# Kernel optimization log

Hardware: AMD Instinct MI355X
Metric: run time of the kernel (lower is better)

## Reference

```python
import jax, jax.numpy as jnp
import numpy as np

CHUNK = 32
EPS = 1e-6

def _l2norm(x):
    return x * jax.lax.rsqrt(jnp.sum(x * x, axis=-1, keepdims=True) + EPS)

def setup_inputs() -> dict:
    key = jax.random.key(0)
    k1, k2, k3, k4 = jax.random.split(key, 4)
    b, h, L, dk, dv = 4, 8, 4096, 128, 128
    return {
        'q': jax.random.normal(k1, (b, h, L, dk), dtype=jnp.float32),
        'k': jax.random.normal(k2, (b, h, L, dk), dtype=jnp.float32),
        'v': jax.random.normal(k3, (b, h, L, dv), dtype=jnp.float32),
        'beta': jax.random.uniform(k4, (b, h, L), dtype=jnp.float32),
    }

def _delta_rule_chunkwise(q, k, v, beta):
    b, h, L, dk = q.shape
    dv = v.shape[-1]
    c = CHUNK
    assert L % c == 0, 'L must be a multiple of chunk_size (no padding path)'
    n = L // c

    q = _l2norm(q)
    k = _l2norm(k)
    v = v * beta[..., None]
    k_beta = k * beta[..., None]

    # [b,h,n,c,d]
    resh = lambda t: t.reshape(b, h, n, c, t.shape[-1])
    qc, kc, vc, kbc = resh(q), resh(k), resh(v), resh(k_beta)

    ones = jnp.ones((c, c), dtype=jnp.float32)
    strict_lower = jnp.tril(ones, -1)      # below diagonal
    lower_inc = jnp.tril(ones, 0)          # diagonal and below

    # inv = -(k_beta @ k^T) with upper-incl-diag zeroed, then forward substitution
    inv = -jnp.einsum('bhncd,bhned->bhnce', kbc, kc) * strict_lower
    for i in range(1, c):
        # inv[..., i, :i] += inv[..., i, :] @ inv[..., :, :i]
        upd = jnp.einsum('bhnk,bhnkj->bhnj', inv[..., i, :], inv[..., :, :i])
        inv = inv.at[..., i, :i].add(upd)
    inv = inv + jnp.eye(c, dtype=inv.dtype)

    u = jnp.einsum('bhnce,bhned->bhncd', inv, vc)    # [b,h,n,c,dv]
    w = jnp.einsum('bhnce,bhned->bhncd', inv, kbc)   # [b,h,n,c,dk]

    # scan over chunks carrying state S [b,h,dk,dv]
    def step(S, inp):
        q_i, k_i, u0_i, w_i = inp  # [b,h,c,d*]
        attn = jnp.einsum('bhcd,bhed->bhce', q_i, k_i) * lower_inc
        u_i = u0_i - jnp.einsum('bhcd,bhdv->bhcv', w_i, S)
        out_i = jnp.einsum('bhcd,bhdv->bhcv', q_i, S) + jnp.einsum('bhce,bhev->bhcv', attn, u_i)
        S = S + jnp.einsum('bhcd,bhcv->bhdv', k_i, u_i)
        return S, out_i

    chunk_first = lambda t: jnp.moveaxis(t, 2, 0)  # [n,b,h,c,d]
    S0 = jnp.zeros((b, h, dk, dv), dtype=q.dtype)
    S, out = jax.lax.scan(step, S0, (chunk_first(qc), chunk_first(kc), chunk_first(u), chunk_first(w)))
    out = jnp.moveaxis(out, 0, 2).reshape(b, h, L, dv)
    return out, S

def reference(q, k, v, beta):
    out, S = _delta_rule_chunkwise(q, k, v, beta)
    return out
```

## Files before the change

### kernel.cpp

```cpp
#include <hip/hip_runtime.h>
#include <math.h>

#define CHUNK 32
#define DK 128
#define DV 128
#define L_SEQ 4096
#define BH 32
#define NCH 128

typedef __attribute__((ext_vector_type(8))) short bf16x8;
typedef __attribute__((ext_vector_type(4))) float f32x4;

union U8 { unsigned int u[4]; bf16x8 v; };

#define MFMA16(a, b, c) __builtin_amdgcn_mfma_f32_16x16x32_bf16((a), (b), (c), 0, 0, 0)
#define LGKM_WAIT() __asm__ __volatile__("s_waitcnt lgkmcnt(0)" ::: "memory")

__device__ __forceinline__ unsigned short f2bf(float x){
    unsigned int u = __builtin_bit_cast(unsigned int, x);
    u = u + 0x7FFFu + ((u >> 16) & 1u);
    return (unsigned short)(u >> 16);
}
__device__ __forceinline__ unsigned int pk2(float a, float b){
    unsigned int r;
    asm("v_cvt_pk_bf16_f32 %0, %1, %2" : "=v"(r) : "v"(a), "v"(b));
    return r;
}

__device__ __forceinline__ bf16x8 afragF32(const float (*M)[36], int row, int q8){
    float4 f0 = *(const float4*)&M[row][q8];
    float4 f1 = *(const float4*)&M[row][q8 + 4];
    U8 t;
    t.u[0] = pk2(f0.x, f0.y); t.u[1] = pk2(f0.z, f0.w);
    t.u[2] = pk2(f1.x, f1.y); t.u[3] = pk2(f1.z, f1.w);
    return t.v;
}
__device__ __forceinline__ bf16x8 bfragF32(const float (*M)[36], int q8, int col){
    U8 t;
#pragma unroll
    for (int j2 = 0; j2 < 4; ++j2)
        t.u[j2] = pk2(M[q8 + 2*j2][col], M[q8 + 2*j2 + 1][col]);
    return t.v;
}


__global__ __launch_bounds__(64, 1)
void prep_kernel(const float* __restrict__ q, const float* __restrict__ k,
                 const float* __restrict__ beta,
                 unsigned short* __restrict__ qw, unsigned short* __restrict__ kw,
                 unsigned short* __restrict__ Tw, unsigned short* __restrict__ Aw)
{
    const int bc = blockIdx.x;
    const size_t row0 = (size_t)bc * CHUNK;
    const int l = threadIdx.x;
    const int r = l & 31, h = l >> 5;
    const int quad = (l >> 4) & 3, ln15 = l & 15, q8 = quad * 8;

    __shared__ unsigned short qn_s[32][136], kn_s[32][136], kb_s[32][136];
    __shared__ float Ms[32][36];
    __shared__ float Rs[32][36];

    const float bet = beta[row0 + r];

    {
        const float4* gp = (const float4*)(q + (row0 + r) * DK + 64 * h);
        float vb[64]; float s = 0.f;
#pragma unroll
        for (int e = 0; e < 16; ++e){
            float4 a = gp[e];
            vb[4*e+0]=a.x; vb[4*e+1]=a.y; vb[4*e+2]=a.z; vb[4*e+3]=a.w;
            s += a.x*a.x + a.y*a.y + a.z*a.z + a.w*a.w;
        }
        s += __shfl_xor(s, 32);
        float sc = rsqrtf(s + 1e-6f);
#pragma unroll
        for (int e = 0; e < 8; ++e){
            U8 t;
#pragma unroll
            for (int j = 0; j < 4; ++j)
                t.u[j] = pk2(vb[8*e+2*j] * sc, vb[8*e+2*j+1] * sc);
            *(bf16x8*)&qn_s[r][64*h + 8*e] = t.v;
            *(bf16x8*)(qw + (row0 + r) * DK + 64*h + 8*e) = t.v;
        }
    }
    {
        const float4* gp = (const float4*)(k + (row0 + r) * DK + 64 * h);
        float vb[64]; float s = 0.f;
#pragma unroll
        for (int e = 0; e < 16; ++e){
            float4 a = gp[e];
            vb[4*e+0]=a.x; vb[4*e+1]=a.y; vb[4*e+2]=a.z; vb[4*e+3]=a.w;
            s += a.x*a.x + a.y*a.y + a.z*a.z + a.w*a.w;
        }
        s += __shfl_xor(s, 32);
        float sc = rsqrtf(s + 1e-6f);
#pragma unroll
        for (int e = 0; e < 8; ++e){
            U8 t, tb;
#pragma unroll
            for (int j = 0; j < 4; ++j){
                float x0 = vb[8*e+2*j] * sc, x1 = vb[8*e+2*j+1] * sc;
                t.u[j]  = pk2(x0, x1);
                tb.u[j] = pk2(x0 * bet, x1 * bet);
            }
            *(bf16x8*)&kn_s[r][64*h + 8*e] = t.v;
            *(bf16x8*)&kb_s[r][64*h + 8*e] = tb.v;
            *(bf16x8*)(kw + (row0 + r) * DK + 64*h + 8*e) = t.v;
        }
    }
    LGKM_WAIT();

    f32x4 Z = {0.f, 0.f, 0.f, 0.f};
    f32x4 Bacc[2][2] = {{Z, Z}, {Z, Z}};
    f32x4 Aacc[2][2] = {{Z, Z}, {Z, Z}};
#pragma unroll
    for (int ks = 0; ks < 4; ++ks){
        bf16x8 bF[2];
        bF[0] = *(const bf16x8*)&kn_s[ln15][32*ks + q8];
        bF[1] = *(const bf16x8*)&kn_s[16 + ln15][32*ks + q8];
#pragma unroll
        for (int mt = 0; mt < 2; ++mt){
            bf16x8 aK = *(const bf16x8*)&kb_s[16*mt + ln15][32*ks + q8];
            bf16x8 aQ = *(const bf16x8*)&qn_s[16*mt + ln15][32*ks + q8];
#pragma unroll
            for (int nt = 0; nt < 2; ++nt){
                Bacc[mt][nt] = MFMA16(aK, bF[nt], Bacc[mt][nt]);
                Aacc[mt][nt] = MFMA16(aQ, bF[nt], Aacc[mt][nt]);
            }
        }
    }

    f32x4 Rc[2][2];
#pragma unroll
    for (int mt = 0; mt < 2; ++mt)
#pragma unroll
    for (int nt = 0; nt < 2; ++nt)
#pragma unroll
    for (int rg = 0; rg < 4; ++rg){
        int row = 16*mt + 4*quad + rg, col = 16*nt + ln15;
        float av = (col <= row) ? Aacc[mt][nt][rg] : 0.f;
        Aw[((size_t)bc << 10) + row*32 + col] = f2bf(av);
        float bm = (col < row) ? -Bacc[mt][nt][rg] : 0.f;
        Ms[row][col] = bm;
        Rc[mt][nt][rg] = bm + ((col == row) ? 1.f : 0.f);
    }

#pragma unroll 1
    for (int rd = 0; rd < 4; ++rd){
        LGKM_WAIT();
        bf16x8 Am[2], Bm2[2];
#pragma unroll
        for (int mt = 0; mt < 2; ++mt) Am[mt] = afragF32(Ms, 16*mt + ln15, q8);
#pragma unroll
        for (int nt = 0; nt < 2; ++nt) Bm2[nt] = bfragF32(Ms, q8, 16*nt + ln15);
        f32x4 Mq[2][2];
#pragma unroll
        for (int mt = 0; mt < 2; ++mt)
#pragma unroll
        for (int nt = 0; nt < 2; ++nt)
            Mq[mt][nt] = MFMA16(Am[mt], Bm2[nt], Z);
#pragma unroll
        for (int mt = 0; mt < 2; ++mt)
#pragma unroll
        for (int nt = 0; nt < 2; ++nt)
#pragma unroll
        for (int rg = 0; rg < 4; ++rg){
            int row = 16*mt + 4*quad + rg, col = 16*nt + ln15;
            Rs[row][col] = Rc[mt][nt][rg];
            Ms[row][col] = Mq[mt][nt][rg];
        }
        LGKM_WAIT();
        bf16x8 Ar[2], Bq[2];
#pragma unroll
        for (int mt = 0; mt < 2; ++mt) Ar[mt] = afragF32(Rs, 16*mt + ln15, q8);
#pragma unroll
        for (int nt = 0; nt < 2; ++nt) Bq[nt] = bfragF32(Ms, q8, 16*nt + ln15);
#pragma unroll
        for (int mt = 0; mt < 2; ++mt)
#pragma unroll
        for (int nt = 0; nt < 2; ++nt)
            Rc[mt][nt] = MFMA16(Ar[mt], Bq[nt], Rc[mt][nt]);
    }

#pragma unroll
    for (int mt = 0; mt < 2; ++mt)
#pragma unroll
    for (int nt = 0; nt < 2; ++nt)
#pragma unroll
    for (int rg = 0; rg < 4; ++rg){
        int row = 16*mt + 4*quad + rg, col = 16*nt + ln15;
        Tw[((size_t)bc << 10) + row*32 + col] = f2bf(Rc[mt][nt][rg]);
    }
}


__global__ __launch_bounds__(64, 1)
void scan_kernel(const float* __restrict__ v, const float* __restrict__ beta,
                 const unsigned short* __restrict__ qw, const unsigned short* __restrict__ kw,
                 const unsigned short* __restrict__ Tw, const unsigned short* __restrict__ Aw,
                 float* __restrict__ out)
{
    const int id = blockIdx.x;
    const int bh = id & 31, cb = id >> 5, c0 = cb * 16;
    const int l = threadIdx.x;
    const int quad = (l >> 4) & 3, ln15 = l & 15, q8 = quad * 8;
    const int hi = l >> 5;

    __shared__ unsigned short knR[4392];
    __shared__ unsigned short Xt[16][40];
    __shared__ unsigned short ut[16][40];

    const f32x4 Z = {0.f, 0.f, 0.f, 0.f};
    f32x4 Sacc[8];
#pragma unroll
    for (int t = 0; t < 8; ++t) Sacc[t] = Z;

    const size_t bhL = (size_t)bh * L_SEQ;
    const int a0 = (((l & 16) << 1) | ln15) << 2;
    const int a1 = a0 + 64;

    bf16x8 kAa[2][4], kAb[2][4];
    bf16x8 qA[2][4], tA[2], aA[2], knA[8], uB;
    float vr[8], br[8];

    auto loadK = [&](int ch, bf16x8 (&kA)[2][4]){
        const unsigned short* kp = kw + (bhL + (size_t)ch * CHUNK) * DK;
#pragma unroll
        for (int mt = 0; mt < 2; ++mt)
#pragma unroll
        for (int ks = 0; ks < 4; ++ks)
            kA[mt][ks] = *(const bf16x8*)(kp + (16*mt + ln15) * DK + 32*ks + q8);
    };
    auto loadQ = [&](int ch){
        const unsigned short* qp = qw + (bhL + (size_t)ch * CHUNK) * DK;
#pragma unroll
        for (int mt = 0; mt < 2; ++mt)
#pragma unroll
        for (int ks = 0; ks < 4; ++ks)
            qA[mt][ks] = *(const bf16x8*)(qp + (16*mt + ln15) * DK + 32*ks + q8);
    };
    auto loadT = [&](int ch){
        const unsigned short* Tp = Tw + ((size_t)(bh * NCH + ch) << 10);
#pragma unroll
        for (int mt = 0; mt < 2; ++mt)
            tA[mt] = *(const bf16x8*)(Tp + (16*mt + ln15) * 32 + q8);
    };
    auto loadA = [&](int ch){
        const unsigned short* Ap = Aw + ((size_t)(bh * NCH + ch) << 10);
#pragma unroll
        for (int mt = 0; mt < 2; ++mt)
            aA[mt] = *(const bf16x8*)(Ap + (16*mt + ln15) * 32 + q8);
    };
    auto loadVB = [&](int ch){
        const size_t row0 = bhL + (size_t)ch * CHUNK;
#pragma unroll
        for (int g = 0; g < 8; ++g){
            int i = 16*(g >> 2) + 4*quad + (g & 3);
            vr[g] = v[(row0 + i) * DV + c0 + ln15];
            br[g] = beta[row0 + i];
        }
    };

    loadK(0, kAa);
    loadQ(0); loadT(0); loadA(0); loadVB(0);
    loadK(1, kAb);
    {
        U8 z; z.u[0] = 0u; z.u[1] = 0u; z.u[2] = 0u; z.u[3] = 0u;
        uB = z.v;
#pragma unroll
        for (int t = 0; t < 8; ++t) knA[t] = z.v;
    }

    auto body = [&](int ch, bf16x8 (&cur)[2][4]){
        const size_t row0 = bhL + (size_t)ch * CHUNK;

#pragma unroll
        for (int t = 0; t < 8; ++t)
            Sacc[t] = MFMA16(knA[t], uB, Sacc[t]);

        int P[8][2];
#pragma unroll
        for (int t = 0; t < 8; ++t){
            P[t][0] = (int)pk2(Sacc[t][0], Sacc[t][1]);
            P[t][1] = (int)pk2(Sacc[t][2], Sacc[t][3]);
        }
        bf16x8 SB[4];
#pragma unroll
        for (int ks = 0; ks < 4; ++ks){
            U8 sb;
            int e, f;
            e = __builtin_amdgcn_ds_bpermute(a0, P[2*ks][0]);
            f = __builtin_amdgcn_ds_bpermute(a0, P[2*ks+1][0]);
            sb.u[0] = (unsigned)(hi ? f : e);
            e = __builtin_amdgcn_ds_bpermute(a0, P[2*ks][1]);
            f = __builtin_amdgcn_ds_bpermute(a0, P[2*ks+1][1]);
            sb.u[1] = (unsigned)(hi ? f : e);
            e = __builtin_amdgcn_ds_bpermute(a1, P[2*ks][0]);
            f = __builtin_amdgcn_ds_bpermute(a1, P[2*ks+1][0]);
            sb.u[2] = (unsigned)(hi ? f : e);
            e = __builtin_amdgcn_ds_bpermute(a1, P[2*ks][1]);
            f = __builtin_amdgcn_ds_bpermute(a1, P[2*ks+1][1]);
            sb.u[3] = (unsigned)(hi ? f : e);
            SB[ks] = sb.v;
        }

        f32x4 Y[2] = {Z, Z}, Op[2] = {Z, Z};
#pragma unroll
        for (int ks = 0; ks < 4; ++ks)
#pragma unroll
        for (int mt = 0; mt < 2; ++mt){
            Y[mt]  = MFMA16(cur[mt][ks], SB[ks], Y[mt]);
            Op[mt] = MFMA16(qA[mt][ks],  SB[ks], Op[mt]);
        }

#pragma unroll
        for (int mt = 0; mt < 2; ++mt){
            unsigned int w0 = pk2(br[4*mt+0] * (vr[4*mt+0] - Y[mt][0]),
                                  br[4*mt+1] * (vr[4*mt+1] - Y[mt][1]));
            unsigned int w1 = pk2(br[4*mt+2] * (vr[4*mt+2] - Y[mt][2]),
                                  br[4*mt+3] * (vr[4*mt+3] - Y[mt][3]));
            *(unsigned int*)&Xt[ln15][16*mt + 4*quad]     = w0;
            *(unsigned int*)&Xt[ln15][16*mt + 4*quad + 2] = w1;
        }

#pragma unroll
        for (int mt = 0; mt < 2; ++mt)
#pragma unroll
        for (int ks = 0; ks < 4; ++ks){
            int i = 16*mt + ln15;
            int ad = i * 136 + (i >> 3) * 16 + 32*ks + q8;
            *(bf16x8*)&knR[ad] = cur[mt][ks];
        }

        bf16x8 Xb = *(const bf16x8*)&Xt[ln15][q8];

        unsigned int rja[32];
#pragma unroll
        for (int t = 0; t < 4; ++t)
#pragma unroll
        for (int j = 0; j < 8; ++j)
            rja[8*t + j] = knR[(q8 + j) * 136 + ((q8 + j) >> 3) * 16 + 16*t + ln15];

        f32x4 U[2];
#pragma unroll
        for (int mt = 0; mt < 2; ++mt) U[mt] = MFMA16(tA[mt], Xb, Z);

#pragma unroll
        for (int mt = 0; mt < 2; ++mt){
            *(unsigned int*)&ut[ln15][16*mt + 4*quad]     = pk2(U[mt][0], U[mt][1]);
            *(unsigned int*)&ut[ln15][16*mt + 4*quad + 2] = pk2(U[mt][2], U[mt][3]);
        }

#pragma unroll
        for (int t = 0; t < 4; ++t){
            U8 kk;
            kk.u[0] = rja[8*t+0] | (rja[8*t+1] << 16);
            kk.u[1] = rja[8*t+2] | (rja[8*t+3] << 16);
            kk.u[2] = rja[8*t+4] | (rja[8*t+5] << 16);
            kk.u[3] = rja[8*t+6] | (rja[8*t+7] << 16);
            knA[t] = kk.v;
        }

        uB = *(const bf16x8*)&ut[ln15][q8];

        const int chn = (ch + 1 < NCH) ? ch + 1 : NCH - 1;
        const int ch2 = (ch + 2 < NCH) ? ch + 2 : NCH - 1;
        loadQ(chn); loadT(chn); loadVB(chn);
        loadK(ch2, cur);

        unsigned int rjb[32];
#pragma unroll
        for (int t = 0; t < 4; ++t)
#pragma unroll
        for (int j = 0; j < 8; ++j)
            rjb[8*t + j] = knR[(q8 + j) * 136 + ((q8 + j) >> 3) * 16 + 16*(t + 4) + ln15];

        f32x4 O[2];
#pragma unroll
        for (int mt = 0; mt < 2; ++mt) O[mt] = MFMA16(aA[mt], uB, Op[mt]);
#pragma unroll
        for (int mt = 0; mt < 2; ++mt)
#pragma unroll
        for (int rg = 0; rg < 4; ++rg)
            out[(row0 + 16*mt + 4*quad + rg) * DV + c0 + ln15] = O[mt][rg];

#pragma unroll
        for (int t = 0; t < 4; ++t){
            U8 kk;
            kk.u[0] = rjb[8*t+0] | (rjb[8*t+1] << 16);
            kk.u[1] = rjb[8*t+2] | (rjb[8*t+3] << 16);
            kk.u[2] = rjb[8*t+4] | (rjb[8*t+5] << 16);
            kk.u[3] = rjb[8*t+6] | (rjb[8*t+7] << 16);
            knA[t + 4] = kk.v;
        }
        loadA(chn);
    };

    for (int ch = 0; ch < NCH; ch += 2){
        body(ch,     kAa);
        body(ch + 1, kAb);
    }
}


__global__ __launch_bounds__(512, 1)
void deltanet_fused(const float* __restrict__ q, const float* __restrict__ k,
                    const float* __restrict__ v, const float* __restrict__ beta,
                    float* __restrict__ out)
{
    const int bh = blockIdx.x;
    const int tid = threadIdx.x;
    const int n = L_SEQ / CHUNK;

    __shared__ float S[DK][DV + 1];
    __shared__ float qs[CHUNK][DK + 1];
    __shared__ float ks[CHUNK][DK + 1];
    __shared__ float vs[CHUNK][DV + 1];
    __shared__ float kbs[CHUNK][DK + 1];
    __shared__ float T[CHUNK][CHUNK + 1];
    __shared__ float at[CHUNK][CHUNK + 1];
    __shared__ float bet[CHUNK];

    for (int idx = tid; idx < DK * DV; idx += 512)
        S[idx / DV][idx % DV] = 0.f;
    __syncthreads();

    const size_t base_bh = (size_t)bh * L_SEQ;

    for (int ch = 0; ch < n; ++ch){
        const size_t row0 = base_bh + (size_t)ch * CHUNK;
        for (int idx = tid; idx < CHUNK * DK; idx += 512){
            int r = idx >> 7, c = idx & 127;
            size_t g = (row0 + (size_t)r) * DK + c;
            qs[r][c] = q[g]; ks[r][c] = k[g]; vs[r][c] = v[g];
        }
        if (tid < CHUNK) bet[tid] = beta[row0 + tid];
        __syncthreads();
        if (tid < 64){
            int r = tid & 31;
            const float* src = (tid < 32) ? &qs[r][0] : &ks[r][0];
            float s = 0.f;
            for (int d = 0; d < DK; ++d){ float x = src[d]; s += x * x; }
            at[(tid < 32) ? 0 : 1][r] = 1.0f / sqrtf(s + 1e-6f);
        }
        __syncthreads();
        for (int idx = tid; idx < CHUNK * DK; idx += 512){
            int r = idx >> 7, c = idx & 127;
            float qq = qs[r][c] * at[0][r];
            float kk = ks[r][c] * at[1][r];
            float b = bet[r];
            qs[r][c] = qq; ks[r][c] = kk; kbs[r][c] = kk * b; vs[r][c] *= b;
        }
        __syncthreads();
        for (int idx = tid; idx < CHUNK * CHUNK; idx += 512){
            int i = idx >> 5, j = idx & 31;
            float s = 0.f;
            if (j < i){
                for (int d = 0; d < DK; ++d) s += kbs[i][d] * ks[j][d];
                s = -s;
            }
            T[i][j] = s;
        }
        __syncthreads();
        for (int i = 1; i < CHUNK; ++i){
            float upd = 0.f;
            if (tid < i){
                int j = tid;
                for (int kk = j + 1; kk < i; ++kk) upd += T[i][kk] * T[kk][j];
            }
            __syncthreads();
            if (tid < i) T[i][tid] += upd;
            __syncthreads();
        }
        if (tid < CHUNK) T[tid][tid] = 1.0f;
        __syncthreads();
        {
            int c = tid & 127;
            int i0 = (tid >> 7) * 8;
            float uacc[8], wacc[8];
#pragma unroll
            for (int r = 0; r < 8; ++r){ uacc[r] = 0.f; wacc[r] = 0.f; }
            for (int j = 0; j < CHUNK; ++j){
                float vvv = vs[j][c], kb = kbs[j][c];
#pragma unroll
                for (int r = 0; r < 8; ++r){
                    float tt = T[i0 + r][j];
                    uacc[r] += tt * vvv; wacc[r] += tt * kb;
                }
            }
            __syncthreads();
#pragma unroll
            for (int r = 0; r < 8; ++r){ vs[i0 + r][c] = uacc[r]; kbs[i0 + r][c] = wacc[r]; }
        }
        __syncthreads();
        for (int idx = tid; idx < CHUNK * CHUNK; idx += 512){
            int i = idx >> 5, j = idx & 31;
            float s = 0.f;
            if (j <= i) for (int d = 0; d < DK; ++d) s += qs[i][d] * ks[j][d];
            at[i][j] = s;
        }
        __syncthreads();
        {
            int c = tid & 127;
            int i0 = (tid >> 7) * 8;
            float acc[8];
#pragma unroll
            for (int r = 0; r < 8; ++r) acc[r] = 0.f;
            for (int d = 0; d < DK; ++d){
                float sv = S[d][c];
#pragma unroll
                for (int r = 0; r < 8; ++r) acc[r] += kbs[i0 + r][d] * sv;
            }
#pragma unroll
            for (int r = 0; r < 8; ++r) vs[i0 + r][c] -= acc[r];
        }
        __syncthreads();
        {
            int c = tid & 127;
            int i0 = (tid >> 7) * 8;
            float acc[8];
#pragma unroll
            for (int r = 0; r < 8; ++r) acc[r] = 0.f;
            for (int d = 0; d < DK; ++d){
                float sv = S[d][c];
#pragma unroll
                for (int r = 0; r < 8; ++r) acc[r] += qs[i0 + r][d] * sv;
            }
            for (int j = 0; j < CHUNK; ++j){
                float uv = vs[j][c];
#pragma unroll
                for (int r = 0; r < 8; ++r) acc[r] += at[i0 + r][j] * uv;
            }
#pragma unroll
            for (int r = 0; r < 8; ++r)
                out[(row0 + (size_t)(i0 + r)) * DV + c] = acc[r];
        }
        __syncthreads();
        {
            int c = tid & 127;
            int d0 = (tid >> 7) * 32;
            float acc[32];
#pragma unroll
            for (int r = 0; r < 32; ++r) acc[r] = 0.f;
            for (int i = 0; i < CHUNK; ++i){
                float uv = vs[i][c];
#pragma unroll
                for (int r = 0; r < 32; ++r) acc[r] += ks[i][d0 + r] * uv;
            }
#pragma unroll
            for (int r = 0; r < 32; ++r) S[d0 + r][c] += acc[r];
        }
        __syncthreads();
    }
}

extern "C" void kernel_launch(void* const* d_in, const int* in_sizes, int n_in,
                              void* d_out, int out_size, void* d_ws, size_t ws_size,
                              hipStream_t stream) {
    const float* q = (const float*)d_in[0];
    const float* k = (const float*)d_in[1];
    const float* v = (const float*)d_in[2];
    const float* beta = (const float*)d_in[3];
    float* out = (float*)d_out;

    const size_t QK = (size_t)BH * L_SEQ * DK;
    const size_t TA = (size_t)BH * NCH * 1024;
    const size_t need = (2 * QK + 2 * TA) * sizeof(unsigned short);

    if (ws_size >= need){
        unsigned short* qwp = (unsigned short*)d_ws;
        unsigned short* kwp = qwp + QK;
        unsigned short* Twp = kwp + QK;
        unsigned short* Awp = Twp + TA;
        prep_kernel<<<BH * NCH, 64, 0, stream>>>(q, k, beta, qwp, kwp, Twp, Awp);
        scan_kernel<<<BH * 8, 64, 0, stream>>>(v, beta, qwp, kwp, Twp, Awp, out);
    } else {
        deltanet_fused<<<BH, 512, 0, stream>>>(q, k, v, beta, out);
    }
}
```

Before: 368.9 us.

## Add register-resident scan kernel with pre-transposed K from prep

The prep kernel now loads q/k straight into MFMA fragment registers instead of staging them in LDS. It also writes an extra transposed bf16 copy of normalized k per chunk. A new scan_fast kernel keeps the state S in MFMA accumulators, moves fragments between lanes with ds_bpermute instead of shared memory, and prefetches the next chunk's operands during the current one. This aims to cut LDS traffic and barriers in the serial chunk scan, at the cost of more workspace and extra global writes and reads for the transposed K, and it only runs when the workspace is large enough.

```diff
diff --git a/kernel.cpp b/kernel.cpp
--- a/kernel.cpp
+++ b/kernel.cpp
@@ -44,90 +44,127 @@
 }
 
 
-__global__ __launch_bounds__(64, 1)
+template<bool WKT>
+__global__ __launch_bounds__(64)
 void prep_kernel(const float* __restrict__ q, const float* __restrict__ k,
                  const float* __restrict__ beta,
                  unsigned short* __restrict__ qw, unsigned short* __restrict__ kw,
-                 unsigned short* __restrict__ Tw, unsigned short* __restrict__ Aw)
+                 unsigned short* __restrict__ Tw, unsigned short* __restrict__ Aw,
+                 unsigned short* __restrict__ kwT)
 {
     const int bc = blockIdx.x;
     const size_t row0 = (size_t)bc * CHUNK;
     const int l = threadIdx.x;
-    const int r = l & 31, h = l >> 5;
     const int quad = (l >> 4) & 3, ln15 = l & 15, q8 = quad * 8;
 
-    __shared__ unsigned short qn_s[32][136], kn_s[32][136], kb_s[32][136];
     __shared__ float Ms[32][36];
     __shared__ float Rs[32][36];
-
-    const float bet = beta[row0 + r];
-
+    __shared__ unsigned short knS[WKT ? 4392 : 2];
+
+    const float bet0 = beta[row0 + ln15];
+    const float bet1 = beta[row0 + 16 + ln15];
+
+    bf16x8 qF[2][4];
     {
-        const float4* gp = (const float4*)(q + (row0 + r) * DK + 64 * h);
-        float vb[64]; float s = 0.f;
-#pragma unroll
-        for (int e = 0; e < 16; ++e){
-            float4 a = gp[e];
-            vb[4*e+0]=a.x; vb[4*e+1]=a.y; vb[4*e+2]=a.z; vb[4*e+3]=a.w;
-            s += a.x*a.x + a.y*a.y + a.z*a.z + a.w*a.w;
-        }
-        s += __shfl_xor(s, 32);
-        float sc = rsqrtf(s + 1e-6f);
-#pragma unroll
-        for (int e = 0; e < 8; ++e){
-            U8 t;
-#pragma unroll
-            for (int j = 0; j < 4; ++j)
-                t.u[j] = pk2(vb[8*e+2*j] * sc, vb[8*e+2*j+1] * sc);
-            *(bf16x8*)&qn_s[r][64*h + 8*e] = t.v;
-            *(bf16x8*)(qw + (row0 + r) * DK + 64*h + 8*e) = t.v;
-        }
-    }
+        float4 raw[2][4][2];
+        float s0 = 0.f, s1 = 0.f;
+#pragma unroll
+        for (int mt = 0; mt < 2; ++mt)
+#pragma unroll
+        for (int ks = 0; ks < 4; ++ks){
+            const float* p = q + (row0 + 16*mt + ln15) * DK + 32*ks + q8;
+            raw[mt][ks][0] = *(const float4*)p;
+            raw[mt][ks][1] = *(const float4*)(p + 4);
+        }
+#pragma unroll
+        for (int ks = 0; ks < 4; ++ks)
+#pragma unroll
+        for (int h = 0; h < 2; ++h){
+            float4 a = raw[0][ks][h], b = raw[1][ks][h];
+            s0 += a.x*a.x + a.y*a.y + a.z*a.z + a.w*a.w;
+            s1 += b.x*b.x + b.y*b.y + b.z*b.z + b.w*b.w;
+        }
+        s0 += __shfl_xor(s0, 16); s0 += __shfl_xor(s0, 32);
+        s1 += __shfl_xor(s1, 16); s1 += __shfl_xor(s1, 32);
+        float sc0 = rsqrtf(s0 + 1e-6f), sc1 = rsqrtf(s1 + 1e-6f);
+#pragma unroll
+        for (int mt = 0; mt < 2; ++mt){
+            float sc = mt ? sc1 : sc0;
+#pragma unroll
+            for (int ks = 0; ks < 4; ++ks){
+                float4 a = raw[mt][ks][0], b = raw[mt][ks][1];
+                U8 t;
+                t.u[0] = pk2(a.x*sc, a.y*sc); t.u[1] = pk2(a.z*sc, a.w*sc);
+                t.u[2] = pk2(b.x*sc, b.y*sc); t.u[3] = pk2(b.z*sc, b.w*sc);
+                qF[mt][ks] = t.v;
+                *(bf16x8*)(qw + (row0 + 16*mt + ln15) * DK + 32*ks + q8) = t.v;
+            }
+        }
+    }
+    bf16x8 kF[2][4], kB[2][4];
     {
-        const float4* gp = (const float4*)(k + (row0 + r) * DK + 64 * h);
-        float vb[64]; float s = 0.f;
-#pragma unroll
-        for (int e = 0; e < 16; ++e){
-            float4 a = gp[e];
-            vb[4*e+0]=a.x; vb[4*e+1]=a.y; vb[4*e+2]=a.z; vb[4*e+3]=a.w;
-            s += a.x*a.x + a.y*a.y + a.z*a.z + a.w*a.w;
-        }
-        s += __shfl_xor(s, 32);
-        float sc = rsqrtf(s + 1e-6f);
-#pragma unroll
-        for (int e = 0; e < 8; ++e){
-            U8 t, tb;
-#pragma unroll
-            for (int j = 0; j < 4; ++j){
-                float x0 = vb[8*e+2*j] * sc, x1 = vb[8*e+2*j+1] * sc;
-                t.u[j]  = pk2(x0, x1);
-                tb.u[j] = pk2(x0 * bet, x1 * bet);
+        float4 raw[2][4][2];
+        float s0 = 0.f, s1 = 0.f;
+#pragma unroll
+        for (int mt = 0; mt < 2; ++mt)
+#pragma unroll
+        for (int ks = 0; ks < 4; ++ks){
+            const float* p = k + (row0 + 16*mt + ln15) * DK + 32*ks + q8;
+            raw[mt][ks][0] = *(const float4*)p;
+            raw[mt][ks][1] = *(const float4*)(p + 4);
+        }
+#pragma unroll
+        for (int ks = 0; ks < 4; ++ks)
+#pragma unroll
+        for (int h = 0; h < 2; ++h){
+            float4 a = raw[0][ks][h], b = raw[1][ks][h];
+            s0 += a.x*a.x + a.y*a.y + a.z*a.z + a.w*a.w;
+            s1 += b.x*b.x + b.y*b.y + b.z*b.z + b.w*b.w;
+        }
+        s0 += __shfl_xor(s0, 16); s0 += __shfl_xor(s0, 32);
+        s1 += __shfl_xor(s1, 16); s1 += __shfl_xor(s1, 32);
+        float sc0 = rsqrtf(s0 + 1e-6f), sc1 = rsqrtf(s1 + 1e-6f);
+#pragma unroll
+        for (int mt = 0; mt < 2; ++mt){
+            float sc = mt ? sc1 : sc0;
+            float bb = mt ? bet1 : bet0;
+#pragma unroll
+            for (int ks = 0; ks < 4; ++ks){
+                float4 a = raw[mt][ks][0], b = raw[mt][ks][1];
+                float x0=a.x*sc, x1=a.y*sc, x2=a.z*sc, x3=a.w*sc;
+                float x4=b.x*sc, x5=b.y*sc, x6=b.z*sc, x7=b.w*sc;
+                U8 t, tb;
+                t.u[0]=pk2(x0,x1); t.u[1]=pk2(x2,x3); t.u[2]=pk2(x4,x5); t.u[3]=pk2(x6,x7);
+                tb.u[0]=pk2(x0*bb,x1*bb); tb.u[1]=pk2(x2*bb,x3*bb);
+                tb.u[2]=pk2(x4*bb,x5*bb); tb.u[3]=pk2(x6*bb,x7*bb);
+                kF[mt][ks] = t.v; kB[mt][ks] = tb.v;
+                *(bf16x8*)(kw + (row0 + 16*mt + ln15) * DK + 32*ks + q8) = t.v;
             }
-            *(bf16x8*)&kn_s[r][64*h + 8*e] = t.v;
-            *(bf16x8*)&kb_s[r][64*h + 8*e] = tb.v;
-            *(bf16x8*)(kw + (row0 + r) * DK + 64*h + 8*e) = t.v;
-        }
-    }
-    LGKM_WAIT();
+        }
+    }
+
+    if constexpr (WKT){
+#pragma unroll
+        for (int mt = 0; mt < 2; ++mt)
+#pragma unroll
+        for (int ks = 0; ks < 4; ++ks){
+            int i = 16*mt + ln15;
+            int ad = i * 136 + (i >> 3) * 16 + 32*ks + q8;
+            *(bf16x8*)&knS[ad] = kF[mt][ks];
+        }
+    }
 
     f32x4 Z = {0.f, 0.f, 0.f, 0.f};
     f32x4 Bacc[2][2] = {{Z, Z}, {Z, Z}};
     f32x4 Aacc[2][2] = {{Z, Z}, {Z, Z}};
 #pragma unroll
-    for (int ks = 0; ks < 4; ++ks){
-        bf16x8 bF[2];
-        bF[0] = *(const bf16x8*)&kn_s[ln15][32*ks + q8];
-        bF[1] = *(const bf16x8*)&kn_s[16 + ln15][32*ks + q8];
-#pragma unroll
-        for (int mt = 0; mt < 2; ++mt){
-            bf16x8 aK = *(const bf16x8*)&kb_s[16*mt + ln15][32*ks + q8];
-            bf16x8 aQ = *(const bf16x8*)&qn_s[16*mt + ln15][32*ks + q8];
-#pragma unroll
-            for (int nt = 0; nt < 2; ++nt){
-                Bacc[mt][nt] = MFMA16(aK, bF[nt], Bacc[mt][nt]);
-                Aacc[mt][nt] = MFMA16(aQ, bF[nt], Aacc[mt][nt]);
-            }
-        }
+    for (int ks = 0; ks < 4; ++ks)
+#pragma unroll
+    for (int mt = 0; mt < 2; ++mt)
+#pragma unroll
+    for (int nt = 0; nt < 2; ++nt){
+        Bacc[mt][nt] = MFMA16(kB[mt][ks], kF[nt][ks], Bacc[mt][nt]);
+        Aacc[mt][nt] = MFMA16(qF[mt][ks], kF[nt][ks], Aacc[mt][nt]);
     }
 
     f32x4 Rc[2][2];
@@ -145,6 +182,23 @@
         Rc[mt][nt][rg] = bm + ((col == row) ? 1.f : 0.f);
     }
 
+    if constexpr (WKT){
+        unsigned short* kT = kwT + ((size_t)bc << 12);
+#pragma unroll
+        for (int t = 0; t < 8; ++t){
+            unsigned short rj[8];
+#pragma unroll
+            for (int j = 0; j < 8; ++j)
+                rj[j] = knS[(q8 + j) * 136 + ((q8 + j) >> 3) * 16 + 16*t + ln15];
+            U8 kk;
+            kk.u[0] = (unsigned)rj[0] | ((unsigned)rj[1] << 16);
+            kk.u[1] = (unsigned)rj[2] | ((unsigned)rj[3] << 16);
+            kk.u[2] = (unsigned)rj[4] | ((unsigned)rj[5] << 16);
+            kk.u[3] = (unsigned)rj[6] | ((unsigned)rj[7] << 16);
+            *(bf16x8*)(kT + (16*t + ln15) * 32 + q8) = kk.v;
+        }
+    }
+
 #pragma unroll 1
     for (int rd = 0; rd < 4; ++rd){
         LGKM_WAIT();
@@ -190,6 +244,166 @@
     for (int rg = 0; rg < 4; ++rg){
         int row = 16*mt + 4*quad + rg, col = 16*nt + ln15;
         Tw[((size_t)bc << 10) + row*32 + col] = f2bf(Rc[mt][nt][rg]);
+    }
+}
+
+
+__global__ __launch_bounds__(64, 1)
+void scan_fast(const float* __restrict__ v, const float* __restrict__ beta,
+               const unsigned short* __restrict__ qw, const unsigned short* __restrict__ kw,
+               const unsigned short* __restrict__ kwT,
+               const unsigned short* __restrict__ Tw, const unsigned short* __restrict__ Aw,
+               float* __restrict__ out)
+{
+    const int id = blockIdx.x;
+    const int bh = id & 31, cb = id >> 5, c0 = cb * 16;
+    const int l = threadIdx.x;
+    const int quad = (l >> 4) & 3, ln15 = l & 15, q8 = quad * 8;
+    const int hi = l >> 5;
+
+    const f32x4 Z = {0.f, 0.f, 0.f, 0.f};
+    f32x4 Sacc[8];
+#pragma unroll
+    for (int t = 0; t < 8; ++t) Sacc[t] = Z;
+
+    const size_t bhL = (size_t)bh * L_SEQ;
+    const int a0 = (((l & 16) << 1) | ln15) << 2;
+    const int a1 = a0 + 64;
+
+    bf16x8 cur[2][4], qA[2][4], knA[8], tA[2], aA[2], uB;
+    float vr[8], br[8];
+
+    auto quadswap = [&](int p0, int p1, int p2, int p3) -> bf16x8 {
+        U8 r; int e, f;
+        e = __builtin_amdgcn_ds_bpermute(a0, p0); f = __builtin_amdgcn_ds_bpermute(a0, p2);
+        r.u[0] = (unsigned)(hi ? f : e);
+        e = __builtin_amdgcn_ds_bpermute(a0, p1); f = __builtin_amdgcn_ds_bpermute(a0, p3);
+        r.u[1] = (unsigned)(hi ? f : e);
+        e = __builtin_amdgcn_ds_bpermute(a1, p0); f = __builtin_amdgcn_ds_bpermute(a1, p2);
+        r.u[2] = (unsigned)(hi ? f : e);
+        e = __builtin_amdgcn_ds_bpermute(a1, p1); f = __builtin_amdgcn_ds_bpermute(a1, p3);
+        r.u[3] = (unsigned)(hi ? f : e);
+        return r.v;
+    };
+
+    auto loadK = [&](int ch){
+        const unsigned short* kp = kw + (bhL + (size_t)ch * CHUNK) * DK;
+#pragma unroll
+        for (int mt = 0; mt < 2; ++mt)
+#pragma unroll
+        for (int ks = 0; ks < 4; ++ks)
+            cur[mt][ks] = *(const bf16x8*)(kp + (16*mt + ln15) * DK + 32*ks + q8);
+    };
+    auto loadQ = [&](int ch){
+        const unsigned short* qp = qw + (bhL + (size_t)ch * CHUNK) * DK;
+#pragma unroll
+        for (int mt = 0; mt < 2; ++mt)
+#pragma unroll
+        for (int ks = 0; ks < 4; ++ks)
+            qA[mt][ks] = *(const bf16x8*)(qp + (16*mt + ln15) * DK + 32*ks + q8);
+    };
+    auto loadT = [&](int ch){
+        const unsigned short* Tp = Tw + ((size_t)(bh * NCH + ch) << 10);
+#pragma unroll
+        for (int mt = 0; mt < 2; ++mt)
+            tA[mt] = *(const bf16x8*)(Tp + (16*mt + ln15) * 32 + q8);
+    };
+    auto loadA = [&](int ch){
+        const unsigned short* Ap = Aw + ((size_t)(bh * NCH + ch) << 10);
+#pragma unroll
+        for (int mt = 0; mt < 2; ++mt)
+            aA[mt] = *(const bf16x8*)(Ap + (16*mt + ln15) * 32 + q8);
+    };
+    auto loadVB = [&](int ch){
+        const size_t row0 = bhL + (size_t)ch * CHUNK;
+#pragma unroll
+        for (int g = 0; g < 8; ++g){
+            int i = 16*(g >> 2) + 4*quad + (g & 3);
+            vr[g] = v[(row0 + i) * DV + c0 + ln15];
+            br[g] = beta[row0 + i];
+        }
+    };
+    auto loadKT = [&](int ch){
+        const unsigned short* p = kwT + ((size_t)(bh * NCH + ch) << 12);
+#pragma unroll
+        for (int t = 0; t < 8; ++t)
+            knA[t] = *(const bf16x8*)(p + (16*t + ln15) * 32 + q8);
+    };
+
+    loadK(0); loadQ(0); loadT(0); loadA(0); loadVB(0);
+    {
+        U8 z; z.u[0] = 0u; z.u[1] = 0u; z.u[2] = 0u; z.u[3] = 0u;
+        uB = z.v;
+#pragma unroll
+        for (int t = 0; t < 8; ++t) knA[t] = z.v;
+    }
+
+    for (int ch = 0; ch < NCH; ++ch){
+        const size_t row0 = bhL + (size_t)ch * CHUNK;
+        const int chn = (ch + 1 < NCH) ? ch + 1 : NCH - 1;
+
+#pragma unroll
+        for (int t = 0; t < 8; ++t)
+            Sacc[t] = MFMA16(knA[t], uB, Sacc[t]);
+
+        loadKT(ch);
+
+        int P[8][2];
+#pragma unroll
+        for (int t = 0; t < 8; ++t){
+            P[t][0] = (int)pk2(Sacc[t][0], Sacc[t][1]);
+            P[t][1] = (int)pk2(Sacc[t][2], Sacc[t][3]);
+        }
+        bf16x8 SB[4];
+#pragma unroll
+        for (int ks = 0; ks < 4; ++ks)
+            SB[ks] = quadswap(P[2*ks][0], P[2*ks][1], P[2*ks+1][0], P[2*ks+1][1]);
+
+        f32x4 Y[2] = {Z, Z}, Op[2] = {Z, Z};
+#pragma unroll
+        for (int ks = 0; ks < 4; ++ks)
+#pragma unroll
+        for (int mt = 0; mt < 2; ++mt){
+            Y[mt]  = MFMA16(cur[mt][ks], SB[ks], Y[mt]);
+            Op[mt] = MFMA16(qA[mt][ks],  SB[ks], Op[mt]);
+        }
+
+        loadK(chn); loadQ(chn);
+
+        int PX0, PX1, PX2, PX3;
+        {
+            float x00 = br[0]*(vr[0]-Y[0][0]), x01 = br[1]*(vr[1]-Y[0][1]);
+            float x02 = br[2]*(vr[2]-Y[0][2]), x03 = br[3]*(vr[3]-Y[0][3]);
+            float x10 = br[4]*(vr[4]-Y[1][0]), x11 = br[5]*(vr[5]-Y[1][1]);
+            float x12 = br[6]*(vr[6]-Y[1][2]), x13 = br[7]*(vr[7]-Y[1][3]);
+            PX0 = (int)pk2(x00, x01); PX1 = (int)pk2(x02, x03);
+            PX2 = (int)pk2(x10, x11); PX3 = (int)pk2(x12, x13);
+        }
+        bf16x8 Xb = quadswap(PX0, PX1, PX2, PX3);
+
+        f32x4 U[2];
+#pragma unroll
+        for (int mt = 0; mt < 2; ++mt) U[mt] = MFMA16(tA[mt], Xb, Z);
+
+        loadT(chn);
+
+        {
+            int PU0 = (int)pk2(U[0][0], U[0][1]), PU1 = (int)pk2(U[0][2], U[0][3]);
+            int PU2 = (int)pk2(U[1][0], U[1][1]), PU3 = (int)pk2(U[1][2], U[1][3]);
+            uB = quadswap(PU0, PU1, PU2, PU3);
+        }
+
+        f32x4 O[2];
+#pragma unroll
+        for (int mt = 0; mt < 2; ++mt) O[mt] = MFMA16(aA[mt], uB, Op[mt]);
+#pragma unroll
+        for (int mt = 0; mt < 2; ++mt)
+#pragma unroll
+        for (int rg = 0; rg < 4; ++rg)
+            out[(row0 + 16*mt + 4*quad + rg) * DV + c0 + ln15] = O[mt][rg];
+
+        loadA(chn);
+        loadVB(chn);
     }
 }
 
@@ -565,14 +779,23 @@
 
     const size_t QK = (size_t)BH * L_SEQ * DK;
     const size_t TA = (size_t)BH * NCH * 1024;
-    const size_t need = (2 * QK + 2 * TA) * sizeof(unsigned short);
-
-    if (ws_size >= need){
+    const size_t need_full = (3 * QK + 2 * TA) * sizeof(unsigned short);
+    const size_t need_mid  = (2 * QK + 2 * TA) * sizeof(unsigned short);
+
+    if (ws_size >= need_full){
         unsigned short* qwp = (unsigned short*)d_ws;
         unsigned short* kwp = qwp + QK;
         unsigned short* Twp = kwp + QK;
         unsigned short* Awp = Twp + TA;
-        prep_kernel<<<BH * NCH, 64, 0, stream>>>(q, k, beta, qwp, kwp, Twp, Awp);
+        unsigned short* kTp = Awp + TA;
+        prep_kernel<true><<<BH * NCH, 64, 0, stream>>>(q, k, beta, qwp, kwp, Twp, Awp, kTp);
+        scan_fast<<<BH * 8, 64, 0, stream>>>(v, beta, qwp, kwp, kTp, Twp, Awp, out);
+    } else if (ws_size >= need_mid){
+        unsigned short* qwp = (unsigned short*)d_ws;
+        unsigned short* kwp = qwp + QK;
+        unsigned short* Twp = kwp + QK;
+        unsigned short* Awp = Twp + TA;
+        prep_kernel<false><<<BH * NCH, 64, 0, stream>>>(q, k, beta, qwp, kwp, Twp, Awp, nullptr);
         scan_kernel<<<BH * 8, 64, 0, stream>>>(v, beta, qwp, kwp, Twp, Awp, out);
     } else {
         deltanet_fused<<<BH, 512, 0, stream>>>(q, k, v, beta, out);
```

After: 364.9 us. About the same (-1.1%).
